# Kernel tuning notes

Hardware: AMD Instinct MI355X
Metric: run time of the kernel (lower is better)

Reference implementation:

```python
import jax, jax.numpy as jnp
import numpy as np

EPS = 1e-6

def _rmsnorm(x, w):
    var = jnp.mean(x * x, axis=-1, keepdims=True)
    return x * jax.lax.rsqrt(var + EPS) * w

def setup_inputs() -> dict:
    key = jax.random.key(0)
    ks = jax.random.split(key, 10)
    B, S, D = 2, 2048, 1024
    H, E, F = 16, 8, 4096
    std = 0.02
    return {
        "x": jax.random.normal(ks[0], (B, S, D), dtype=jnp.float32),
        "ln1_w": jnp.ones((D,), dtype=jnp.float32),
        "ln2_w": jnp.ones((D,), dtype=jnp.float32),
        "wq": jax.random.normal(ks[1], (D, D), dtype=jnp.float32) * std,
        "wk": jax.random.normal(ks[2], (D, D), dtype=jnp.float32) * std,
        "wv": jax.random.normal(ks[3], (D, D), dtype=jnp.float32) * std,
        "wo": jax.random.normal(ks[4], (D, D), dtype=jnp.float32) * std,
        "wr": jax.random.normal(ks[5], (D, E), dtype=jnp.float32) * std,
        "w1": jax.random.normal(ks[6], (E, D, F), dtype=jnp.float32) * std,
        "w2": jax.random.normal(ks[7], (E, F, D), dtype=jnp.float32) * std,
    }

def reference(x, ln1_w, ln2_w, wq, wk, wv, wo, wr, w1, w2):
    B, S, D = x.shape
    H = 16
    Dh = D // H
    E = wr.shape[1]
    K = 2
    Z_COEF = 0.001

    # --- bidirectional attention sublayer ---
    residual = x
    xn = _rmsnorm(x, ln1_w)
    q = (xn @ wq).reshape(B, S, H, Dh).transpose(0, 2, 1, 3)  # [B,H,S,Dh]
    k = (xn @ wk).reshape(B, S, H, Dh).transpose(0, 2, 1, 3)
    v = (xn @ wv).reshape(B, S, H, Dh).transpose(0, 2, 1, 3)
    scale = 1.0 / jnp.sqrt(jnp.asarray(Dh, dtype=x.dtype))
    scores = jnp.einsum("bhqd,bhkd->bhqk", q, k) * scale  # non-causal
    attn = jax.nn.softmax(scores, axis=-1)
    ctx = jnp.einsum("bhqk,bhkd->bhqd", attn, v)
    attn_out = ctx.transpose(0, 2, 1, 3).reshape(B, S, D) @ wo
    x = residual + attn_out

    # --- MoE sublayer ---
    residual = x
    xn2 = _rmsnorm(x, ln2_w)
    logits = xn2 @ wr                       # [B,S,E]
    probs = jax.nn.softmax(logits, axis=-1)
    topv, topi = jax.lax.top_k(probs, K)    # [B,S,K]
    weights = topv / jnp.sum(topv, axis=-1, keepdims=True)
    onehot = jax.nn.one_hot(topi, E, dtype=x.dtype)          # [B,S,K,E]
    dispatch = jnp.sum(onehot * weights[..., None], axis=-2)  # [B,S,E] combine weights

    # router losses: switch-style load balance + z-loss
    frac_tokens = jnp.mean(jnp.sum(onehot, axis=-2), axis=(0, 1))  # [E]
    frac_probs = jnp.mean(probs, axis=(0, 1))                      # [E]
    aux_loss = E * jnp.sum(frac_tokens * frac_probs) / K
    z = jax.nn.logsumexp(logits, axis=-1)
    router_loss = aux_loss + Z_COEF * jnp.mean(z * z)

    # expert-grouped FFN: dense per expert, masked combine (loop over fixed E)
    expert_out = jnp.zeros_like(xn2)
    for e in range(E):
        h = jax.nn.gelu(xn2 @ w1[e])
        expert_out = expert_out + dispatch[..., e:e + 1] * (h @ w2[e])

    out = residual + expert_out
    return out, router_loss
```

## Files before the change

kernel.cpp:

```cpp
#include <hip/hip_runtime.h>
#include <hip/hip_bf16.h>
#include <math.h>
#include <stdint.h>

#define DEV static __device__ __forceinline__

typedef __attribute__((ext_vector_type(8))) short short8;
typedef __attribute__((ext_vector_type(8))) unsigned short ushort8;
typedef __attribute__((ext_vector_type(4))) float floatx4;

using bf16 = __hip_bfloat16;

constexpr int Bc = 2, Sc = 2048, Dc = 1024, Hc = 16, DHc = 64, Ec = 8, Fc = 4096;
constexpr int Tc = Bc * Sc;

DEV floatx4 mfma_bf16(short8 a, short8 b, floatx4 c) {
  return __builtin_amdgcn_mfma_f32_16x16x32_bf16(a, b, c, 0, 0, 0);
}

DEV float gelu_tanh(float x) {
  float z = 0.7978845608028654f * (x + 0.044715f * x * x * x);
  z = fminf(fmaxf(z, -15.f), 15.f);
  float t = __expf(2.f * z);
  return 0.5f * x * (1.f + (t - 1.f) / (t + 1.f));
}

DEV void gl16(const void* g, void* l) {
  __builtin_amdgcn_global_load_lds(
      reinterpret_cast<const __attribute__((address_space(1))) void*>(
          reinterpret_cast<uintptr_t>(g)),
      reinterpret_cast<__attribute__((address_space(3))) void*>(
          reinterpret_cast<uintptr_t>(l)),
      16, 0, 0);
}

DEV void tr_tile(const float* __restrict__ W, bf16* __restrict__ Wt,
                 int K, int N, bf16 (*Ts)[72]) {
  const int n0 = blockIdx.x * 64, k0 = blockIdx.y * 64;
  const int tid = threadIdx.x;
#pragma unroll
  for (int it = 0; it < 4; it++) {
    int u = tid + it * 256;
    int r = u >> 4, c4 = (u & 15) << 2;
    floatx4 v = *(const floatx4*)(W + (size_t)(k0 + r) * N + n0 + c4);
#pragma unroll
    for (int j = 0; j < 4; j++) Ts[c4 + j][r] = __float2bfloat16(v[j]);
  }
  __syncthreads();
#pragma unroll
  for (int it = 0; it < 2; it++) {
    int u = tid + it * 256;
    int rn = u >> 3, kc = (u & 7) << 3;
    *(short8*)(Wt + (size_t)(n0 + rn) * K + k0 + kc) = *(const short8*)(&Ts[rn][kc]);
  }
}

__global__ __launch_bounds__(256) void k_wt(const float* __restrict__ W,
                                            bf16* __restrict__ Wt, int K, int N) {
  __shared__ __align__(16) bf16 Ts[64][72];
  const size_t mb = (size_t)blockIdx.z * K * N;
  tr_tile(W + mb, Wt + mb, K, N, Ts);
}

__global__ __launch_bounds__(256) void k_wt4(
    const float* __restrict__ a, const float* __restrict__ b,
    const float* __restrict__ c, const float* __restrict__ d,
    bf16* __restrict__ o) {
  __shared__ __align__(16) bf16 Ts[64][72];
  const int z = blockIdx.z;
  const float* W = z == 0 ? a : (z == 1 ? b : (z == 2 ? c : d));
  tr_tile(W, o + (size_t)z * Dc * Dc, Dc, Dc, Ts);
}

DEV void gemm_core(bf16* As, bf16* Bs,
                   const bf16* __restrict__ A, int lda, int m0,
                   const bf16* __restrict__ Bt, int ldb, int n0,
                   int Kdim, floatx4 (&acc)[4][4]) {
  const int tid = threadIdx.x;
  const int lane = tid & 63;
  const int wave = tid >> 6;
  const int wm = wave & 1, wn = wave >> 1;
  const int l15 = lane & 15, quad = lane >> 4;

#pragma unroll
  for (int mi = 0; mi < 4; mi++)
#pragma unroll
    for (int ni = 0; ni < 4; ni++)
#pragma unroll
      for (int r = 0; r < 4; r++) acc[mi][ni][r] = 0.f;

  const int srow0 = tid >> 2;
  const int sg = tid & 3;
  const int sw = ((quad ^ ((l15 >> 1) & 3)) << 3);
  const int nK = Kdim >> 5;

  for (int kb = 0; kb < nK; kb++) {
    const int k0 = kb << 5;
    __syncthreads();
#pragma unroll
    for (int it = 0; it < 2; it++) {
      const int row = srow0 + it * 64;
      const int sk = k0 + ((sg ^ ((row >> 1) & 3)) << 3);
      const int lbase = (it * 256 + wave * 64) * 8;
      gl16(A + (size_t)(m0 + row) * lda + sk, As + lbase);
      gl16(Bt + (size_t)(n0 + row) * ldb + sk, Bs + lbase);
    }
    __syncthreads();
    short8 af[4], bfr[4];
#pragma unroll
    for (int mi = 0; mi < 4; mi++)
      af[mi] = *(const short8*)(As + (wm * 64 + mi * 16 + l15) * 32 + sw);
#pragma unroll
    for (int ni = 0; ni < 4; ni++)
      bfr[ni] = *(const short8*)(Bs + (wn * 64 + ni * 16 + l15) * 32 + sw);
#pragma unroll
    for (int mi = 0; mi < 4; mi++)
#pragma unroll
      for (int ni = 0; ni < 4; ni++)
        acc[mi][ni] = mfma_bf16(af[mi], bfr[ni], acc[mi][ni]);
  }
}

#define GEMM_SHARED \
  __shared__ __align__(16) bf16 As[128 * 32]; \
  __shared__ __align__(16) bf16 Bs[128 * 32];
#define LANE_DECODE \
  const int tid = threadIdx.x; const int lane = tid & 63; const int wave = tid >> 6; \
  const int wm = wave & 1, wn = wave >> 1; const int l15 = lane & 15, quad = lane >> 4; \
  (void)tid; (void)lane;
#define XCD_SWZ(GX, GY) \
  int bx, by; { \
    constexpr int nwg = (GX) * (GY); \
    int flat = blockIdx.y * (GX) + blockIdx.x; \
    int wg = (flat & 7) * (nwg >> 3) + (flat >> 3); \
    bx = wg % (GX); by = wg / (GX); }

__global__ __launch_bounds__(256) void k_rms(const float* __restrict__ x,
                                             const float* __restrict__ w,
                                             bf16* __restrict__ out,
                                             float* __restrict__ outf) {
  __shared__ float red[4];
  const int tid = threadIdx.x, lane = tid & 63, wave = tid >> 6;
  const size_t base = (size_t)blockIdx.x * Dc + tid * 4;
  floatx4 v = *(const floatx4*)(x + base);
  float ss = v[0] * v[0] + v[1] * v[1] + v[2] * v[2] + v[3] * v[3];
#pragma unroll
  for (int off = 32; off >= 1; off >>= 1) ss += __shfl_xor(ss, off);
  if (lane == 0) red[wave] = ss;
  __syncthreads();
  float tot = red[0] + red[1] + red[2] + red[3];
  float rr = rsqrtf(tot * (1.f / Dc) + 1e-6f);
  floatx4 wv = *(const floatx4*)(w + tid * 4);
  floatx4 res;
#pragma unroll
  for (int j = 0; j < 4; j++) res[j] = v[j] * rr * wv[j];
#pragma unroll
  for (int j = 0; j < 4; j++) out[base + j] = __float2bfloat16(res[j]);
  if (outf) *(floatx4*)(outf + base) = res;
}

__global__ __launch_bounds__(256, 4) void k_gemm_qkv(
    const bf16* __restrict__ xn, const bf16* __restrict__ wt,
    bf16* __restrict__ q, bf16* __restrict__ k, bf16* __restrict__ v) {
  GEMM_SHARED; LANE_DECODE;
  XCD_SWZ(Dc / 128, Tc / 128);
  const bf16* W = wt + (size_t)blockIdx.z * Dc * Dc;
  bf16* out = blockIdx.z == 0 ? q : (blockIdx.z == 1 ? k : v);
  const int m0 = by * 128, n0 = bx * 128;
  floatx4 acc[4][4];
  gemm_core(As, Bs, xn, Dc, m0, W, Dc, n0, Dc, acc);
#pragma unroll
  for (int mi = 0; mi < 4; mi++)
#pragma unroll
    for (int ni = 0; ni < 4; ni++)
#pragma unroll
      for (int r = 0; r < 4; r++) {
        int row = m0 + wm * 64 + mi * 16 + quad * 4 + r;
        int col = n0 + wn * 64 + ni * 16 + l15;
        int b = row >> 11, s = row & 2047, h = col >> 6, dh = col & 63;
        out[((((size_t)b * Hc + h) * Sc + s) << 6) + dh] = __float2bfloat16(acc[mi][ni][r]);
      }
}

__global__ __launch_bounds__(256, 4) void k_gemm_wo(
    const bf16* __restrict__ ctx, const bf16* __restrict__ wot,
    const float* __restrict__ x, float* __restrict__ x1) {
  GEMM_SHARED; LANE_DECODE;
  XCD_SWZ(Dc / 128, Tc / 128);
  const int m0 = by * 128, n0 = bx * 128;
  floatx4 acc[4][4];
  gemm_core(As, Bs, ctx, Dc, m0, wot, Dc, n0, Dc, acc);
#pragma unroll
  for (int mi = 0; mi < 4; mi++)
#pragma unroll
    for (int ni = 0; ni < 4; ni++)
#pragma unroll
      for (int r = 0; r < 4; r++) {
        int row = m0 + wm * 64 + mi * 16 + quad * 4 + r;
        int col = n0 + wn * 64 + ni * 16 + l15;
        size_t idx = (size_t)row * Dc + col;
        x1[idx] = acc[mi][ni][r] + x[idx];
      }
}

__global__ __launch_bounds__(256) void k_attn(
    const bf16* __restrict__ Q, const bf16* __restrict__ K,
    const bf16* __restrict__ V, bf16* __restrict__ ctx) {
  __shared__ __align__(16) bf16 Ks[32 * 72];
  __shared__ __align__(16) bf16 Vs[64 * 40];
  __shared__ __align__(16) bf16 Ps[4 * 16 * 40];
  const int tid = threadIdx.x, lane = tid & 63, wave = tid >> 6;
  const int l15 = lane & 15, quad = lane >> 4;
  const int bh = blockIdx.y;
  const size_t base = (size_t)bh * Sc * DHc;
  const bf16* Qb = Q + base; const bf16* Kb = K + base; const bf16* Vb = V + base;
  const int q0 = blockIdx.x * 64 + wave * 16;
  bf16* Pw = Ps + wave * (16 * 40);

  short8 aq[2];
#pragma unroll
  for (int kk2 = 0; kk2 < 2; kk2++)
    aq[kk2] = *(const short8*)(Qb + (size_t)(q0 + l15) * 64 + kk2 * 32 + quad * 8);

  float m_i[4], l_i[4];
  floatx4 o[4];
#pragma unroll
  for (int r = 0; r < 4; r++) { m_i[r] = -__builtin_inff(); l_i[r] = 0.f; }
#pragma unroll
  for (int n4 = 0; n4 < 4; n4++)
#pragma unroll
    for (int r = 0; r < 4; r++) o[n4][r] = 0.f;

  for (int kt = 0; kt < Sc / 32; kt++) {
    const int kb = kt * 32;
    __syncthreads();
    {
      int row = tid >> 3, kc = (tid & 7) << 3;
      *(short8*)(Ks + row * 72 + kc) = *(const short8*)(Kb + (size_t)(kb + row) * 64 + kc);
    }
    if (tid < 128) {
      int kp = tid >> 3, dg = tid & 7;
      ushort8 a0 = *(const ushort8*)(Vb + (size_t)(kb + 2 * kp) * 64 + dg * 8);
      ushort8 a1 = *(const ushort8*)(Vb + (size_t)(kb + 2 * kp + 1) * 64 + dg * 8);
#pragma unroll
      for (int j = 0; j < 8; j++) {
        int dh = dg * 8 + j;
        int elem = dh * 40 + ((((kp >> 2) ^ (dh >> 3)) & 3) << 3) + ((kp & 3) << 1);
        *(unsigned int*)(Vs + elem) = (unsigned int)a0[j] | ((unsigned int)a1[j] << 16);
      }
    }
    __syncthreads();
    floatx4 sc[2];
#pragma unroll
    for (int ni = 0; ni < 2; ni++) {
#pragma unroll
      for (int r = 0; r < 4; r++) sc[ni][r] = 0.f;
#pragma unroll
      for (int kk2 = 0; kk2 < 2; kk2++) {
        short8 bk = *(const short8*)(Ks + (ni * 16 + l15) * 72 + kk2 * 32 + quad * 8);
        sc[ni] = mfma_bf16(aq[kk2], bk, sc[ni]);
      }
    }
#pragma unroll
    for (int ni = 0; ni < 2; ni++)
#pragma unroll
      for (int r = 0; r < 4; r++) sc[ni][r] *= 0.125f;
    float rmax[4];
#pragma unroll
    for (int r = 0; r < 4; r++) rmax[r] = fmaxf(sc[0][r], sc[1][r]);
#pragma unroll
    for (int off = 1; off < 16; off <<= 1)
#pragma unroll
      for (int r = 0; r < 4; r++) rmax[r] = fmaxf(rmax[r], __shfl_xor(rmax[r], off));
    float alpha[4], rsum[4];
#pragma unroll
    for (int r = 0; r < 4; r++) {
      float nm = fmaxf(m_i[r], rmax[r]);
      alpha[r] = __expf(m_i[r] - nm);
      m_i[r] = nm;
    }
#pragma unroll
    for (int ni = 0; ni < 2; ni++)
#pragma unroll
      for (int r = 0; r < 4; r++) sc[ni][r] = __expf(sc[ni][r] - m_i[r]);
#pragma unroll
    for (int r = 0; r < 4; r++) rsum[r] = sc[0][r] + sc[1][r];
#pragma unroll
    for (int off = 1; off < 16; off <<= 1)
#pragma unroll
      for (int r = 0; r < 4; r++) rsum[r] += __shfl_xor(rsum[r], off);
#pragma unroll
    for (int r = 0; r < 4; r++) l_i[r] = l_i[r] * alpha[r] + rsum[r];
#pragma unroll
    for (int n4 = 0; n4 < 4; n4++)
#pragma unroll
      for (int r = 0; r < 4; r++) o[n4][r] *= alpha[r];
#pragma unroll
    for (int ni = 0; ni < 2; ni++)
#pragma unroll
      for (int r = 0; r < 4; r++)
        Pw[(quad * 4 + r) * 40 + ni * 16 + l15] = __float2bfloat16(sc[ni][r]);
    __syncthreads();
    short8 ap = *(const short8*)(Pw + l15 * 40 + quad * 8);
#pragma unroll
    for (int n4 = 0; n4 < 4; n4++) {
      int dh = n4 * 16 + l15;
      short8 bv = *(const short8*)(Vs + dh * 40 + (((quad ^ (dh >> 3)) & 3) << 3));
      o[n4] = mfma_bf16(ap, bv, o[n4]);
    }
  }
  const int b = bh >> 4, h = bh & 15;
#pragma unroll
  for (int n4 = 0; n4 < 4; n4++)
#pragma unroll
    for (int r = 0; r < 4; r++) {
      int s = q0 + quad * 4 + r;
      int d = h * 64 + n4 * 16 + l15;
      ctx[(size_t)(b * Sc + s) * Dc + d] = __float2bfloat16(o[n4][r] / l_i[r]);
    }
}

__global__ __launch_bounds__(256) void k_router(
    const float* __restrict__ xn2f, const float* __restrict__ wr,
    int* __restrict__ topi, float* __restrict__ topw,
    int* __restrict__ counts, float* __restrict__ sum_probs,
    float* __restrict__ sum_z2) {
  __shared__ float sp[8]; __shared__ float sz[1]; __shared__ int scnt[8];
  const int tid = threadIdx.x, wave = tid >> 6, lane = tid & 63;
  if (tid < 8) { sp[tid] = 0.f; scnt[tid] = 0; }
  if (tid == 0) sz[0] = 0.f;
  __syncthreads();
  const int t = blockIdx.x * 4 + wave;
  float a[8];
#pragma unroll
  for (int e = 0; e < 8; e++) a[e] = 0.f;
  const float* xr = xn2f + (size_t)t * Dc;
#pragma unroll 4
  for (int i = 0; i < 16; i++) {
    int d = lane + i * 64;
    float xv = xr[d];
    floatx4 wa = *(const floatx4*)(wr + d * 8);
    floatx4 wb = *(const floatx4*)(wr + d * 8 + 4);
#pragma unroll
    for (int e = 0; e < 4; e++) a[e] += xv * wa[e];
#pragma unroll
    for (int e = 0; e < 4; e++) a[e + 4] += xv * wb[e];
  }
#pragma unroll
  for (int off = 1; off < 64; off <<= 1)
#pragma unroll
    for (int e = 0; e < 8; e++) a[e] += __shfl_xor(a[e], off);
  float mx = a[0];
#pragma unroll
  for (int e = 1; e < 8; e++) mx = fmaxf(mx, a[e]);
  float pr[8], sum = 0.f;
#pragma unroll
  for (int e = 0; e < 8; e++) { pr[e] = __expf(a[e] - mx); sum += pr[e]; }
  float inv = 1.f / sum;
#pragma unroll
  for (int e = 0; e < 8; e++) pr[e] *= inv;
  float lse = mx + logf(sum);
  int i0 = 0; float p0 = pr[0];
#pragma unroll
  for (int e = 1; e < 8; e++) if (pr[e] > p0) { p0 = pr[e]; i0 = e; }
  int i1 = -1; float p1 = -1.f;
#pragma unroll
  for (int e = 0; e < 8; e++) if (e != i0 && pr[e] > p1) { p1 = pr[e]; i1 = e; }
  float wsum = p0 + p1;
  if (lane == 0) {
    topi[2 * t] = i0; topi[2 * t + 1] = i1;
    topw[2 * t] = p0 / wsum; topw[2 * t + 1] = p1 / wsum;
    atomicAdd(&scnt[i0], 1); atomicAdd(&scnt[i1], 1);
#pragma unroll
    for (int e = 0; e < 8; e++) atomicAdd(&sp[e], pr[e]);
    atomicAdd(&sz[0], lse * lse);
  }
  __syncthreads();
  if (tid < 8) { atomicAdd(&counts[tid], scnt[tid]); atomicAdd(&sum_probs[tid], sp[tid]); }
  if (tid == 0) atomicAdd(sum_z2, sz[0]);
}

__global__ void k_meta(const int* __restrict__ counts, int* __restrict__ offs,
                       const float* __restrict__ sum_probs,
                       const float* __restrict__ sum_z2, float* __restrict__ loss_out) {
  float aux = 0.f;
  offs[0] = 0;
  for (int e = 0; e < 8; e++) {
    offs[e + 1] = offs[e] + counts[e];
    aux += ((float)counts[e] / Tc) * (sum_probs[e] / Tc);
  }
  float loss = (float)Ec * aux * 0.5f + 0.001f * (sum_z2[0] / Tc);
  loss_out[0] = loss;
}

__global__ __launch_bounds__(256) void k_gather(
    const bf16* __restrict__ xn2, const int* __restrict__ topi,
    const int* __restrict__ offs, int* __restrict__ cursors,
    int* __restrict__ rowpos, bf16* __restrict__ Ag) {
  const int tid = threadIdx.x, wave = tid >> 6, lane = tid & 63;
  const int t = blockIdx.x * 4 + wave;
  const int i0 = topi[2 * t], i1 = topi[2 * t + 1];
  int r0 = 0, r1 = 0;
  if (lane == 0) {
    r0 = atomicAdd(&cursors[i0], 1);
    r1 = atomicAdd(&cursors[i1], 1);
    rowpos[2 * t] = r0; rowpos[2 * t + 1] = r1;
  }
  r0 = __shfl(r0, 0); r1 = __shfl(r1, 0);
  const short8* src = (const short8*)(xn2 + (size_t)t * Dc);
  short8 c0 = src[lane], c1 = src[lane + 64];
  short8* d0 = (short8*)(Ag + (size_t)(offs[i0] + r0) * Dc);
  short8* d1 = (short8*)(Ag + (size_t)(offs[i1] + r1) * Dc);
  d0[lane] = c0; d0[lane + 64] = c1;
  d1[lane] = c0; d1[lane + 64] = c1;
}

__global__ __launch_bounds__(256, 4) void k_ffn1(
    const bf16* __restrict__ Ag, const bf16* __restrict__ w1t,
    bf16* __restrict__ Hb, const int* __restrict__ offs) {
  const int e = blockIdx.z;
  const int cnt = offs[e + 1] - offs[e];
  const int m0 = blockIdx.y * 128;
  if (m0 >= cnt) return;
  GEMM_SHARED; LANE_DECODE;
  const int n0 = blockIdx.x * 128;
  const bf16* A = Ag + (size_t)offs[e] * Dc;
  const bf16* W = w1t + (size_t)e * Dc * Fc;
  bf16* Hp = Hb + (size_t)offs[e] * Fc;
  floatx4 acc[4][4];
  gemm_core(As, Bs, A, Dc, m0, W, Dc, n0, Dc, acc);
#pragma unroll
  for (int mi = 0; mi < 4; mi++)
#pragma unroll
    for (int ni = 0; ni < 4; ni++)
#pragma unroll
      for (int r = 0; r < 4; r++) {
        int row = m0 + wm * 64 + mi * 16 + quad * 4 + r;
        int col = n0 + wn * 64 + ni * 16 + l15;
        if (row < cnt)
          Hp[(size_t)row * Fc + col] = __float2bfloat16(gelu_tanh(acc[mi][ni][r]));
      }
}

__global__ __launch_bounds__(256, 4) void k_ffn2(
    const bf16* __restrict__ Hb, const bf16* __restrict__ w2t,
    float* __restrict__ Ob, const int* __restrict__ offs) {
  const int e = blockIdx.z;
  const int cnt = offs[e + 1] - offs[e];
  const int m0 = blockIdx.y * 128;
  if (m0 >= cnt) return;
  GEMM_SHARED; LANE_DECODE;
  const int n0 = blockIdx.x * 128;
  const bf16* A = Hb + (size_t)offs[e] * Fc;
  const bf16* W = w2t + (size_t)e * Fc * Dc;
  float* Op = Ob + (size_t)offs[e] * Dc;
  floatx4 acc[4][4];
  gemm_core(As, Bs, A, Fc, m0, W, Fc, n0, Fc, acc);
#pragma unroll
  for (int mi = 0; mi < 4; mi++)
#pragma unroll
    for (int ni = 0; ni < 4; ni++)
#pragma unroll
      for (int r = 0; r < 4; r++) {
        int row = m0 + wm * 64 + mi * 16 + quad * 4 + r;
        int col = n0 + wn * 64 + ni * 16 + l15;
        if (row < cnt) Op[(size_t)row * Dc + col] = acc[mi][ni][r];
      }
}

__global__ __launch_bounds__(256) void k_combine(
    const float* __restrict__ x1, const float* __restrict__ Ob,
    const int* __restrict__ topi, const float* __restrict__ topw,
    const int* __restrict__ rowpos, const int* __restrict__ offs,
    float* __restrict__ out) {
  const int t = blockIdx.x, tid = threadIdx.x;
  const int i0 = topi[2 * t], i1 = topi[2 * t + 1];
  const float w0 = topw[2 * t], w1 = topw[2 * t + 1];
  const float* o0 = Ob + (size_t)(offs[i0] + rowpos[2 * t]) * Dc;
  const float* o1 = Ob + (size_t)(offs[i1] + rowpos[2 * t + 1]) * Dc;
  const float* xr = x1 + (size_t)t * Dc;
  floatx4 a = *(const floatx4*)(xr + tid * 4);
  floatx4 b = *(const floatx4*)(o0 + tid * 4);
  floatx4 c = *(const floatx4*)(o1 + tid * 4);
  floatx4 res;
#pragma unroll
  for (int j = 0; j < 4; j++) res[j] = a[j] + w0 * b[j] + w1 * c[j];
  *(floatx4*)(out + (size_t)t * Dc + tid * 4) = res;
}

extern "C" void kernel_launch(void* const* d_in, const int* in_sizes, int n_in,
                              void* d_out, int out_size, void* d_ws, size_t ws_size,
                              hipStream_t stream) {
  (void)in_sizes; (void)n_in; (void)out_size; (void)ws_size;
  const float* x    = (const float*)d_in[0];
  const float* ln1w = (const float*)d_in[1];
  const float* ln2w = (const float*)d_in[2];
  const float* wq   = (const float*)d_in[3];
  const float* wk   = (const float*)d_in[4];
  const float* wv   = (const float*)d_in[5];
  const float* wo   = (const float*)d_in[6];
  const float* wr   = (const float*)d_in[7];
  const float* w1   = (const float*)d_in[8];
  const float* w2   = (const float*)d_in[9];
  float* out = (float*)d_out;

  char* p = (char*)d_ws;
  auto take = [&](size_t bytes) {
    char* r = p; p += (bytes + 255) & ~(size_t)255; return r;
  };
  bf16*  xn   = (bf16*)take((size_t)Tc * Dc * 2);
  bf16*  qb   = (bf16*)take((size_t)Tc * Dc * 2);
  bf16*  kb   = (bf16*)take((size_t)Tc * Dc * 2);
  bf16*  vb   = (bf16*)take((size_t)Tc * Dc * 2);
  bf16*  ctx  = (bf16*)take((size_t)Tc * Dc * 2);
  float* x1   = (float*)take((size_t)Tc * Dc * 4);
  bf16*  xn2  = (bf16*)take((size_t)Tc * Dc * 2);
  float* xn2f = (float*)take((size_t)Tc * Dc * 4);
  bf16*  Ag   = (bf16*)take((size_t)2 * Tc * Dc * 2);
  bf16*  Hb   = (bf16*)take((size_t)2 * Tc * Fc * 2);
  float* Ob   = (float*)take((size_t)2 * Tc * Dc * 4);
  bf16*  wtqkvo = (bf16*)take((size_t)4 * Dc * Dc * 2);
  bf16*  wtbig  = (bf16*)take((size_t)Ec * (size_t)Dc * Fc * 2);
  int*   counts    = (int*)take(512);
  int*   cursors   = counts + 8;
  float* sum_probs = (float*)(counts + 16);
  float* sum_z2    = sum_probs + 8;
  int*   offs      = (int*)take(256);
  int*   topi      = (int*)take((size_t)2 * Tc * 4);
  float* topw      = (float*)take((size_t)2 * Tc * 4);
  int*   rowpos    = (int*)take((size_t)2 * Tc * 4);

  hipMemsetAsync(counts, 0, 512, stream);

  k_wt4<<<dim3(Dc / 64, Dc / 64, 4), 256, 0, stream>>>(wq, wk, wv, wo, wtqkvo);
  k_wt<<<dim3(Fc / 64, Dc / 64, Ec), 256, 0, stream>>>(w1, wtbig, Dc, Fc);

  k_rms<<<Tc, 256, 0, stream>>>(x, ln1w, xn, nullptr);
  k_gemm_qkv<<<dim3(Dc / 128, Tc / 128, 3), 256, 0, stream>>>(xn, wtqkvo, qb, kb, vb);
  k_attn<<<dim3(Sc / 64, Bc * Hc), 256, 0, stream>>>(qb, kb, vb, ctx);
  k_gemm_wo<<<dim3(Dc / 128, Tc / 128), 256, 0, stream>>>(ctx, wtqkvo + (size_t)3 * Dc * Dc, x, x1);
  k_rms<<<Tc, 256, 0, stream>>>(x1, ln2w, xn2, xn2f);
  k_router<<<Tc / 4, 256, 0, stream>>>(xn2f, wr, topi, topw, counts, sum_probs, sum_z2);
  k_meta<<<1, 1, 0, stream>>>(counts, offs, sum_probs, sum_z2, out + (size_t)Tc * Dc);
  k_gather<<<Tc / 4, 256, 0, stream>>>(xn2, topi, offs, cursors, rowpos, Ag);
  k_ffn1<<<dim3(Fc / 128, Tc / 128, Ec), 256, 0, stream>>>(Ag, wtbig, Hb, offs);
  k_wt<<<dim3(Dc / 64, Fc / 64, Ec), 256, 0, stream>>>(w2, wtbig, Fc, Dc);
  k_ffn2<<<dim3(Dc / 128, Tc / 128, Ec), 256, 0, stream>>>(Hb, wtbig, Ob, offs);
  k_combine<<<Tc, 256, 0, stream>>>(x1, Ob, topi, topw, rowpos, offs, out);
}
```

Before: 982.6 us.

## Widen attention key tile to 64, use async K loads, fold softmax scale into Q

The flash attention kernel now processes 64 keys per iteration instead of 32. That halves the number of loop iterations and the barriers among them. K tiles are loaded straight into LDS through gl16 with an XOR-swizzled layout, and all 256 threads now help transpose V. The 1/sqrt(Dh) scale is folded into the Q projection epilogue, which removes the per-score multiply. The change uses more LDS and registers per block, which could lower occupancy.

```diff
diff --git a/kernel.cpp b/kernel.cpp
--- a/kernel.cpp
+++ b/kernel.cpp
@@ -166,6 +166,7 @@
   XCD_SWZ(Dc / 128, Tc / 128);
   const bf16* W = wt + (size_t)blockIdx.z * Dc * Dc;
   bf16* out = blockIdx.z == 0 ? q : (blockIdx.z == 1 ? k : v);
+  const float qsc = (blockIdx.z == 0) ? 0.125f : 1.0f;
   const int m0 = by * 128, n0 = bx * 128;
   floatx4 acc[4][4];
   gemm_core(As, Bs, xn, Dc, m0, W, Dc, n0, Dc, acc);
@@ -178,7 +179,8 @@
         int row = m0 + wm * 64 + mi * 16 + quad * 4 + r;
         int col = n0 + wn * 64 + ni * 16 + l15;
         int b = row >> 11, s = row & 2047, h = col >> 6, dh = col & 63;
-        out[((((size_t)b * Hc + h) * Sc + s) << 6) + dh] = __float2bfloat16(acc[mi][ni][r]);
+        out[((((size_t)b * Hc + h) * Sc + s) << 6) + dh] =
+            __float2bfloat16(acc[mi][ni][r] * qsc);
       }
 }
 
@@ -206,16 +208,16 @@
 __global__ __launch_bounds__(256) void k_attn(
     const bf16* __restrict__ Q, const bf16* __restrict__ K,
     const bf16* __restrict__ V, bf16* __restrict__ ctx) {
-  __shared__ __align__(16) bf16 Ks[32 * 72];
-  __shared__ __align__(16) bf16 Vs[64 * 40];
-  __shared__ __align__(16) bf16 Ps[4 * 16 * 40];
+  __shared__ __align__(16) bf16 Ks[64 * 64];
+  __shared__ __align__(16) bf16 Vs[64 * 72];
+  __shared__ __align__(16) bf16 Ps[4 * 16 * 72];
   const int tid = threadIdx.x, lane = tid & 63, wave = tid >> 6;
   const int l15 = lane & 15, quad = lane >> 4;
   const int bh = blockIdx.y;
   const size_t base = (size_t)bh * Sc * DHc;
   const bf16* Qb = Q + base; const bf16* Kb = K + base; const bf16* Vb = V + base;
   const int q0 = blockIdx.x * 64 + wave * 16;
-  bf16* Pw = Ps + wave * (16 * 40);
+  bf16* Pw = Ps + wave * (16 * 72);
 
   short8 aq[2];
 #pragma unroll
@@ -231,43 +233,47 @@
 #pragma unroll
     for (int r = 0; r < 4; r++) o[n4][r] = 0.f;
 
-  for (int kt = 0; kt < Sc / 32; kt++) {
-    const int kb = kt * 32;
+  const int ksrow = tid >> 3, ksg = tid & 7;
+  const int vkp = tid >> 3, vdg = tid & 7;
+  const int vsg = ((vkp >> 2) ^ vdg) & 7;
+
+  for (int kt = 0; kt < Sc / 64; kt++) {
+    const int kb = kt * 64;
     __syncthreads();
+#pragma unroll
+    for (int it = 0; it < 2; it++) {
+      int row = ksrow + it * 32;
+      gl16(Kb + (size_t)(kb + row) * 64 + ((ksg ^ (row & 7)) << 3),
+           Ks + (it * 256 + wave * 64) * 8);
+    }
     {
-      int row = tid >> 3, kc = (tid & 7) << 3;
-      *(short8*)(Ks + row * 72 + kc) = *(const short8*)(Kb + (size_t)(kb + row) * 64 + kc);
-    }
-    if (tid < 128) {
-      int kp = tid >> 3, dg = tid & 7;
-      ushort8 a0 = *(const ushort8*)(Vb + (size_t)(kb + 2 * kp) * 64 + dg * 8);
-      ushort8 a1 = *(const ushort8*)(Vb + (size_t)(kb + 2 * kp + 1) * 64 + dg * 8);
+      ushort8 a0 = *(const ushort8*)(Vb + (size_t)(kb + 2 * vkp) * 64 + vdg * 8);
+      ushort8 a1 = *(const ushort8*)(Vb + (size_t)(kb + 2 * vkp + 1) * 64 + vdg * 8);
 #pragma unroll
       for (int j = 0; j < 8; j++) {
-        int dh = dg * 8 + j;
-        int elem = dh * 40 + ((((kp >> 2) ^ (dh >> 3)) & 3) << 3) + ((kp & 3) << 1);
+        int dh = vdg * 8 + j;
+        int elem = dh * 72 + vsg * 8 + (vkp & 3) * 2;
         *(unsigned int*)(Vs + elem) = (unsigned int)a0[j] | ((unsigned int)a1[j] << 16);
       }
     }
     __syncthreads();
-    floatx4 sc[2];
-#pragma unroll
-    for (int ni = 0; ni < 2; ni++) {
+    floatx4 sc[4];
+#pragma unroll
+    for (int ni = 0; ni < 4; ni++) {
 #pragma unroll
       for (int r = 0; r < 4; r++) sc[ni][r] = 0.f;
+      const int key = ni * 16 + l15;
 #pragma unroll
       for (int kk2 = 0; kk2 < 2; kk2++) {
-        short8 bk = *(const short8*)(Ks + (ni * 16 + l15) * 72 + kk2 * 32 + quad * 8);
+        short8 bk = *(const short8*)(Ks + key * 64 +
+                                     (((kk2 * 4 + quad) ^ (key & 7)) << 3));
         sc[ni] = mfma_bf16(aq[kk2], bk, sc[ni]);
       }
     }
-#pragma unroll
-    for (int ni = 0; ni < 2; ni++)
-#pragma unroll
-      for (int r = 0; r < 4; r++) sc[ni][r] *= 0.125f;
     float rmax[4];
 #pragma unroll
-    for (int r = 0; r < 4; r++) rmax[r] = fmaxf(sc[0][r], sc[1][r]);
+    for (int r = 0; r < 4; r++)
+      rmax[r] = fmaxf(fmaxf(sc[0][r], sc[1][r]), fmaxf(sc[2][r], sc[3][r]));
 #pragma unroll
     for (int off = 1; off < 16; off <<= 1)
 #pragma unroll
@@ -280,11 +286,12 @@
       m_i[r] = nm;
     }
 #pragma unroll
-    for (int ni = 0; ni < 2; ni++)
+    for (int ni = 0; ni < 4; ni++)
 #pragma unroll
       for (int r = 0; r < 4; r++) sc[ni][r] = __expf(sc[ni][r] - m_i[r]);
 #pragma unroll
-    for (int r = 0; r < 4; r++) rsum[r] = sc[0][r] + sc[1][r];
+    for (int r = 0; r < 4; r++)
+      rsum[r] = (sc[0][r] + sc[1][r]) + (sc[2][r] + sc[3][r]);
 #pragma unroll
     for (int off = 1; off < 16; off <<= 1)
 #pragma unroll
@@ -296,17 +303,21 @@
 #pragma unroll
       for (int r = 0; r < 4; r++) o[n4][r] *= alpha[r];
 #pragma unroll
-    for (int ni = 0; ni < 2; ni++)
+    for (int ni = 0; ni < 4; ni++)
 #pragma unroll
       for (int r = 0; r < 4; r++)
-        Pw[(quad * 4 + r) * 40 + ni * 16 + l15] = __float2bfloat16(sc[ni][r]);
+        Pw[(quad * 4 + r) * 72 + ni * 16 + l15] = __float2bfloat16(sc[ni][r]);
     __syncthreads();
-    short8 ap = *(const short8*)(Pw + l15 * 40 + quad * 8);
-#pragma unroll
-    for (int n4 = 0; n4 < 4; n4++) {
-      int dh = n4 * 16 + l15;
-      short8 bv = *(const short8*)(Vs + dh * 40 + (((quad ^ (dh >> 3)) & 3) << 3));
-      o[n4] = mfma_bf16(ap, bv, o[n4]);
+#pragma unroll
+    for (int kk = 0; kk < 2; kk++) {
+      short8 ap = *(const short8*)(Pw + l15 * 72 + kk * 32 + quad * 8);
+#pragma unroll
+      for (int n4 = 0; n4 < 4; n4++) {
+        int dh = n4 * 16 + l15;
+        short8 bv = *(const short8*)(Vs + dh * 72 +
+                                     ((((kk * 4 + quad) ^ (dh >> 3)) & 7) << 3));
+        o[n4] = mfma_bf16(ap, bv, o[n4]);
+      }
     }
   }
   const int b = bh >> 4, h = bh & 15;
```

Result: faster. 930.9 us (-5.3%).
